# Kernel tuning notes

Hardware: AMD Instinct MI355X
Metric: run time of the kernel (lower is better)

Reference implementation:

```python
import jax, jax.numpy as jnp
import numpy as np
from jax.ops import segment_sum

N_NODES = 100000
N_EDGES = 3200000
N_GRAPHS = 64


def gcn_conv(x, src, dst, W, b, num_nodes):
    h = x @ W  # [N, H]
    loop = jnp.arange(num_nodes, dtype=src.dtype)
    s = jnp.concatenate([src, loop])
    d = jnp.concatenate([dst, loop])
    deg = segment_sum(jnp.ones_like(d, dtype=h.dtype), d, num_segments=num_nodes)
    dinv = jnp.where(deg > 0, jax.lax.rsqrt(deg), 0.0)
    norm = dinv[s] * dinv[d]  # [E+N]
    msgs = h[s] * norm[:, None]  # gather + scale
    out = segment_sum(msgs, d, num_segments=num_nodes)  # scatter-add to targets
    return out + b


def setup_inputs() -> dict:
    key = jax.random.key(0)
    ks = jax.random.split(key, 8)
    F_IN, H, C = 128, 256, 2
    x = jax.random.normal(ks[0], (N_NODES, F_IN), dtype=jnp.float32)
    edge_index = jax.random.randint(ks[1], (2, N_EDGES), 0, N_NODES, dtype=jnp.int64)
    batch = jnp.sort(jax.random.randint(ks[2], (N_NODES,), 0, N_GRAPHS, dtype=jnp.int64))
    W1 = jax.random.normal(ks[3], (F_IN, H), dtype=jnp.float32) / np.sqrt(F_IN)
    b1 = jnp.zeros((H,), dtype=jnp.float32)
    W2 = jax.random.normal(ks[4], (H, H), dtype=jnp.float32) / np.sqrt(H)
    b2 = jnp.zeros((H,), dtype=jnp.float32)
    fc_w = jax.random.normal(ks[5], (H, C), dtype=jnp.float32) / np.sqrt(H)
    fc_b = jnp.zeros((C,), dtype=jnp.float32)
    return {"x": x, "edge_index": edge_index, "batch": batch, "W1": W1, "b1": b1,
            "W2": W2, "b2": b2, "fc_w": fc_w, "fc_b": fc_b}


def reference(x, edge_index, batch, W1, b1, W2, b2, fc_w, fc_b):
    src, dst = edge_index[0], edge_index[1]
    n = x.shape[0]
    h = jax.nn.relu(gcn_conv(x, src, dst, W1, b1, n))
    h = jax.nn.relu(gcn_conv(h, src, dst, W2, b2, n))
    # global_mean_pool over graph ids
    sums = segment_sum(h, batch, num_segments=N_GRAPHS)  # [G, H]
    cnts = segment_sum(jnp.ones((n,), dtype=h.dtype), batch, num_segments=N_GRAPHS)
    pooled = sums / jnp.maximum(cnts, 1.0)[:, None]
    logits = pooled @ fc_w + fc_b
    return jax.nn.log_softmax(logits, axis=1)
```

## Files before the change

### kernel.cpp

```cpp
#include <hip/hip_runtime.h>
#include <cstdint>

#define N_NODES 100000
#define N_EDGES 3200000
#define N_GRAPHS 64
#define HDIM 256
#define F_IN 128

#define BUCKET_BITS 7
#define NPB 128
#define N_BUCKETS ((N_NODES + NPB - 1) / NPB)
#define CHUNK 8192
#define NCHUNK ((N_EDGES + CHUNK - 1) / CHUNK)

typedef __attribute__((ext_vector_type(8))) short bf16x8;
typedef __attribute__((ext_vector_type(4))) float f32x4;
typedef __attribute__((ext_vector_type(2))) float f32x2;

__device__ __forceinline__ unsigned short f2bf(float f) {
    unsigned int b = __float_as_uint(f);
    b = (b + 0x7FFFu + ((b >> 16) & 1u)) >> 16;
    return (unsigned short)b;
}

__device__ __forceinline__ unsigned int pack4_fp8(float a, float b, float c, float d) {
    int v = 0;
    v = __builtin_amdgcn_cvt_pk_fp8_f32(a, b, v, false);
    v = __builtin_amdgcn_cvt_pk_fp8_f32(c, d, v, true);
    return (unsigned int)v;
}
__device__ __forceinline__ unsigned char pack1_fp8(float a) {
    int v = __builtin_amdgcn_cvt_pk_fp8_f32(a, a, 0, false);
    return (unsigned char)(v & 0xFF);
}

__global__ void zero_f(float* p, int n) {
    int i = blockIdx.x * blockDim.x + threadIdx.x;
    if (i < n) p[i] = 0.0f;
}

__global__ __launch_bounds__(256) void block_count(const int* __restrict__ dst,
                                                   int* __restrict__ counts, int nE) {
    __shared__ int hist[N_BUCKETS];
    int blk = blockIdx.x, t = threadIdx.x;
    for (int i = t; i < N_BUCKETS; i += 256) hist[i] = 0;
    __syncthreads();
    int lo = blk * CHUNK;
    int hi = lo + CHUNK < nE ? lo + CHUNK : nE;
    for (int i = lo + t; i < hi; i += 256) atomicAdd(&hist[dst[i] >> BUCKET_BITS], 1);
    __syncthreads();
    for (int i = t; i < N_BUCKETS; i += 256) counts[blk * N_BUCKETS + i] = hist[i];
}

__global__ __launch_bounds__(256) void bucket_totals(const int* __restrict__ counts,
                                                     int* __restrict__ tot) {
    __shared__ int red[256];
    int b = blockIdx.x, t = threadIdx.x;
    int s = 0;
    for (int blk = t; blk < NCHUNK; blk += 256) s += counts[blk * N_BUCKETS + b];
    red[t] = s;
    __syncthreads();
    for (int o = 128; o > 0; o >>= 1) {
        if (t < o) red[t] += red[t + o];
        __syncthreads();
    }
    if (t == 0) tot[b] = red[0];
}

__global__ __launch_bounds__(1024) void scan_buckets(const int* __restrict__ tot,
                                                     int* __restrict__ base, int nb) {
    __shared__ int lds[1024];
    int t = threadIdx.x;
    int v = (t < nb) ? tot[t] : 0;
    lds[t] = v;
    __syncthreads();
    for (int off = 1; off < 1024; off <<= 1) {
        int a = (t >= off) ? lds[t - off] : 0;
        __syncthreads();
        lds[t] += a;
        __syncthreads();
    }
    int excl = lds[t] - v;
    if (t < nb) base[t] = excl;
    if (t == nb) base[t] = excl;
}

__global__ __launch_bounds__(512) void column_scan(const int* __restrict__ counts,
                                                   const int* __restrict__ base,
                                                   int* __restrict__ offs) {
    __shared__ int lds[512];
    int b = blockIdx.x, t = threadIdx.x;
    int v = (t < NCHUNK) ? counts[t * N_BUCKETS + b] : 0;
    lds[t] = v;
    __syncthreads();
    for (int off = 1; off < 512; off <<= 1) {
        int a = (t >= off) ? lds[t - off] : 0;
        __syncthreads();
        lds[t] += a;
        __syncthreads();
    }
    if (t < NCHUNK) offs[t * N_BUCKETS + b] = base[b] + lds[t] - v;
}

__global__ __launch_bounds__(256) void block_scatter(const int* __restrict__ src,
                                                     const int* __restrict__ dst,
                                                     const int* __restrict__ offs,
                                                     unsigned int* __restrict__ rec, int nE) {
    __shared__ int cur[N_BUCKETS];
    int blk = blockIdx.x, t = threadIdx.x;
    for (int i = t; i < N_BUCKETS; i += 256) cur[i] = offs[blk * N_BUCKETS + i];
    __syncthreads();
    int lo = blk * CHUNK;
    int hi = lo + CHUNK < nE ? lo + CHUNK : nE;
    for (int i = lo + t; i < hi; i += 256) {
        int d = dst[i];
        int b = d >> BUCKET_BITS;
        int pos = atomicAdd(&cur[b], 1);
        rec[pos] = (unsigned int)src[i] | ((unsigned int)(d & (NPB - 1)) << 17);
    }
}

__global__ __launch_bounds__(512) void bucket_csr(const unsigned int* __restrict__ rec,
                                                  const int* __restrict__ base,
                                                  int* __restrict__ ptr, float* __restrict__ dinv,
                                                  int* __restrict__ csr_src, int n) {
    __shared__ int hist[NPB];
    __shared__ int sc[NPB];
    __shared__ int cur[NPB];
    int b = blockIdx.x;
    int lo = base[b], hi = base[b + 1];
    int t = threadIdx.x;
    if (t < NPB) hist[t] = 0;
    __syncthreads();
    for (int i = lo + t; i < hi; i += 512) atomicAdd(&hist[rec[i] >> 17], 1);
    __syncthreads();
    if (t < NPB) sc[t] = hist[t];
    __syncthreads();
    for (int off = 1; off < NPB; off <<= 1) {
        int a = (t < NPB && t >= off) ? sc[t - off] : 0;
        __syncthreads();
        if (t < NPB) sc[t] += a;
        __syncthreads();
    }
    if (t < NPB) {
        int node = b * NPB + t;
        int incl = sc[t];
        int excl = incl - hist[t];
        if (node < n) {
            ptr[node] = lo + incl;
            dinv[node] = rsqrtf((float)hist[t] + 1.0f);
        }
        cur[t] = lo + excl;
    }
    __syncthreads();
    for (int i = lo + t; i < hi; i += 512) {
        unsigned int r = rec[i];
        int pos = atomicAdd(&cur[r >> 17], 1);
        csr_src[pos] = (int)(r & 0x1FFFFu);
    }
}

__global__ void convert_x_pre(const float* __restrict__ x, const float* __restrict__ dinv,
                              unsigned int* __restrict__ xp, int n) {
    int tid = blockIdx.x * blockDim.x + threadIdx.x;
    if (tid >= n * (F_IN / 4)) return;
    int node = tid / (F_IN / 4);
    float di = dinv[node];
    float4 v = ((const float4*)x)[tid];
    xp[tid] = pack4_fp8(v.x * di, v.y * di, v.z * di, v.w * di);
}

__global__ void pack_w(const float* __restrict__ W, unsigned short* __restrict__ hi,
                       unsigned short* __restrict__ lo, int K) {
    int idx = blockIdx.x * blockDim.x + threadIdx.x;
    if (idx >= K * HDIM) return;
    int k = idx >> 8, c = idx & 255;
    float w = W[idx];
    unsigned short h = f2bf(w);
    float hf = __uint_as_float((unsigned int)h << 16);
    unsigned short l = f2bf(w - hf);
    int pos = ((k >> 5) * 16 + (c >> 4)) * 512 + ((((k >> 3) & 3) * 16) + (c & 15)) * 8 + (k & 7);
    hi[pos] = h;
    lo[pos] = l;
}

__global__ void csr_agg128_fp8(const unsigned char* __restrict__ h, const int* __restrict__ ptr,
                               const int* __restrict__ csr, const float* __restrict__ dinv,
                               unsigned short* __restrict__ out, int n) {
    int wave = threadIdx.x >> 6, lane = threadIdx.x & 63;
    int node = blockIdx.x * 4 + wave;
    if (node >= n) return;
    int begin = node ? ptr[node - 1] : 0;
    int end = ptr[node];
    unsigned int u = *(const unsigned short*)(h + (size_t)node * 128 + lane * 2);
    f32x2 v = __builtin_amdgcn_cvt_pk_f32_fp8((int)u, false);
    float a0 = v.x, a1 = v.y;
    int i = begin;
    for (; i + 8 <= end; i += 8) {
        unsigned int uu[8];
#pragma unroll
        for (int j = 0; j < 8; j++) {
            int s = csr[i + j];
            uu[j] = *(const unsigned short*)(h + (size_t)s * 128 + lane * 2);
        }
#pragma unroll
        for (int j = 0; j < 8; j++) {
            f32x2 d = __builtin_amdgcn_cvt_pk_f32_fp8((int)uu[j], false);
            a0 += d.x; a1 += d.y;
        }
    }
    for (; i < end; i++) {
        int s = csr[i];
        unsigned int u0 = *(const unsigned short*)(h + (size_t)s * 128 + lane * 2);
        f32x2 d = __builtin_amdgcn_cvt_pk_f32_fp8((int)u0, false);
        a0 += d.x; a1 += d.y;
    }
    float dn = dinv[node];
    unsigned int o = (unsigned int)f2bf(a0 * dn) | ((unsigned int)f2bf(a1 * dn) << 16);
    *(unsigned int*)(out + (size_t)node * 128 + lane * 2) = o;
}

__global__ void csr_agg256_fp8(const unsigned char* __restrict__ h, const int* __restrict__ ptr,
                               const int* __restrict__ csr, const float* __restrict__ dinv,
                               unsigned short* __restrict__ out, int n) {
    int wave = threadIdx.x >> 6, lane = threadIdx.x & 63;
    int node = blockIdx.x * 4 + wave;
    if (node >= n) return;
    int begin = node ? ptr[node - 1] : 0;
    int end = ptr[node];
    unsigned int u = *(const unsigned int*)(h + (size_t)node * 256 + lane * 4);
    f32x2 vl = __builtin_amdgcn_cvt_pk_f32_fp8((int)u, false);
    f32x2 vh = __builtin_amdgcn_cvt_pk_f32_fp8((int)u, true);
    float a0 = vl.x, a1 = vl.y, a2 = vh.x, a3 = vh.y;
    int i = begin;
    for (; i + 8 <= end; i += 8) {
        unsigned int uu[8];
#pragma unroll
        for (int j = 0; j < 8; j++) {
            int s = csr[i + j];
            uu[j] = *(const unsigned int*)(h + (size_t)s * 256 + lane * 4);
        }
#pragma unroll
        for (int j = 0; j < 8; j++) {
            f32x2 dl = __builtin_amdgcn_cvt_pk_f32_fp8((int)uu[j], false);
            f32x2 dh = __builtin_amdgcn_cvt_pk_f32_fp8((int)uu[j], true);
            a0 += dl.x; a1 += dl.y; a2 += dh.x; a3 += dh.y;
        }
    }
    for (; i < end; i++) {
        int s = csr[i];
        unsigned int u0 = *(const unsigned int*)(h + (size_t)s * 256 + lane * 4);
        f32x2 dl = __builtin_amdgcn_cvt_pk_f32_fp8((int)u0, false);
        f32x2 dh = __builtin_amdgcn_cvt_pk_f32_fp8((int)u0, true);
        a0 += dl.x; a1 += dl.y; a2 += dh.x; a3 += dh.y;
    }
    float dn = dinv[node];
    uint2 o;
    o.x = (unsigned int)f2bf(a0 * dn) | ((unsigned int)f2bf(a1 * dn) << 16);
    o.y = (unsigned int)f2bf(a2 * dn) | ((unsigned int)f2bf(a3 * dn) << 16);
    *(uint2*)(out + (size_t)node * 256 + lane * 4) = o;
}

template <int K, bool PRESCALE>
__global__ __launch_bounds__(256, 3) void gemm_mfma(
    const unsigned short* __restrict__ A, const unsigned short* __restrict__ Whi,
    const unsigned short* __restrict__ Wlo, const float* __restrict__ bias,
    const float* __restrict__ dinv, void* __restrict__ outp, int n) {
    int wave = threadIdx.x >> 6, lane = threadIdx.x & 63;
    int quad = lane >> 4, l16 = lane & 15;
    int rowgrp = wave >> 1, colhalf = wave & 1;
    int rowbase = blockIdx.x * 64 + rowgrp * 32;

    f32x4 acc[2][8];
#pragma unroll
    for (int s = 0; s < 2; s++)
#pragma unroll
        for (int ct = 0; ct < 8; ct++) acc[s][ct] = (f32x4){0.f, 0.f, 0.f, 0.f};

    int r0 = rowbase + l16;
    int r1 = rowbase + 16 + l16;
    int rc0 = r0 < n ? r0 : n - 1;
    int rc1 = r1 < n ? r1 : n - 1;

    for (int kt = 0; kt < K / 32; kt++) {
        bf16x8 a0 = *(const bf16x8*)(A + (size_t)rc0 * K + kt * 32 + quad * 8);
        bf16x8 a1 = *(const bf16x8*)(A + (size_t)rc1 * K + kt * 32 + quad * 8);
        const unsigned short* wh = Whi + ((size_t)kt * 16 + colhalf * 8) * 512 + lane * 8;
        const unsigned short* wl = Wlo + ((size_t)kt * 16 + colhalf * 8) * 512 + lane * 8;
#pragma unroll
        for (int ct = 0; ct < 8; ct++) {
            bf16x8 bh = *(const bf16x8*)(wh + ct * 512);
            bf16x8 bl = *(const bf16x8*)(wl + ct * 512);
            acc[0][ct] = __builtin_amdgcn_mfma_f32_16x16x32_bf16(a0, bh, acc[0][ct], 0, 0, 0);
            acc[0][ct] = __builtin_amdgcn_mfma_f32_16x16x32_bf16(a0, bl, acc[0][ct], 0, 0, 0);
            acc[1][ct] = __builtin_amdgcn_mfma_f32_16x16x32_bf16(a1, bh, acc[1][ct], 0, 0, 0);
            acc[1][ct] = __builtin_amdgcn_mfma_f32_16x16x32_bf16(a1, bl, acc[1][ct], 0, 0, 0);
        }
    }

#pragma unroll
    for (int s = 0; s < 2; s++) {
#pragma unroll
        for (int ct = 0; ct < 8; ct++) {
            int col = colhalf * 128 + ct * 16 + l16;
            float b = bias[col];
#pragma unroll
            for (int r = 0; r < 4; r++) {
                int row = rowbase + s * 16 + quad * 4 + r;
                if (row < n) {
                    float v = acc[s][ct][r] + b;
                    v = v > 0.0f ? v : 0.0f;
                    if (PRESCALE) {
                        ((unsigned char*)outp)[(size_t)row * HDIM + col] = pack1_fp8(v * dinv[row]);
                    } else {
                        ((float*)outp)[(size_t)row * HDIM + col] = v;
                    }
                }
            }
        }
    }
}

__global__ void pool_sum_runs(const float* __restrict__ h, const int* __restrict__ batch,
                              float* __restrict__ pool, float* __restrict__ cnt, int n) {
    constexpr int ROWS = 128;
    int f = threadIdx.x;
    int r0 = blockIdx.x * ROWS;
    int rend = r0 + ROWS;
    if (rend > n) rend = n;
    float acc = 0.0f;
    int cur = batch[r0];
    int runlen = 0;
    for (int r = r0; r < rend; r++) {
        int g = batch[r];
        if (g != cur) {
            atomicAdd(&pool[cur * HDIM + f], acc);
            if (f == 0) atomicAdd(&cnt[cur], (float)runlen);
            acc = 0.0f; runlen = 0; cur = g;
        }
        acc += h[(size_t)r * HDIM + f];
        runlen++;
    }
    atomicAdd(&pool[cur * HDIM + f], acc);
    if (f == 0) atomicAdd(&cnt[cur], (float)runlen);
}

__global__ void final_head(const float* __restrict__ pool, const float* __restrict__ cnt,
                           const float* __restrict__ fcw, const float* __restrict__ fcb,
                           float* __restrict__ out) {
    int g = threadIdx.x;
    if (g < N_GRAPHS) {
        float c = cnt[g];
        c = c > 1.0f ? c : 1.0f;
        float inv = 1.0f / c;
        float l0 = fcb[0], l1 = fcb[1];
        for (int f = 0; f < HDIM; f++) {
            float p = pool[g * HDIM + f] * inv;
            l0 += p * fcw[f * 2 + 0];
            l1 += p * fcw[f * 2 + 1];
        }
        float m = fmaxf(l0, l1);
        float lse = m + logf(expf(l0 - m) + expf(l1 - m));
        out[g * 2 + 0] = l0 - lse;
        out[g * 2 + 1] = l1 - lse;
    }
}

extern "C" void kernel_launch(void* const* d_in, const int* in_sizes, int n_in,
                              void* d_out, int out_size, void* d_ws, size_t ws_size,
                              hipStream_t stream) {
    const float* x = (const float*)d_in[0];
    const int* ei = (const int*)d_in[1];
    const int* batch = (const int*)d_in[2];
    const float* W1 = (const float*)d_in[3];
    const float* b1 = (const float*)d_in[4];
    const float* W2 = (const float*)d_in[5];
    const float* b2 = (const float*)d_in[6];
    const float* fcw = (const float*)d_in[7];
    const float* fcb = (const float*)d_in[8];
    float* out = (float*)d_out;

    const int* src = ei;
    const int* dst = ei + N_EDGES;

    char* ws = (char*)d_ws;
    float* dinv = (float*)ws;            ws += 4 * ((N_NODES + 255) & ~255);
    int* ptr = (int*)ws;                 ws += 4 * ((N_NODES + 255) & ~255);
    int* csr_src = (int*)ws;             ws += 4 * (size_t)N_EDGES;
    int* counts = (int*)ws;              ws += 4 * (size_t)NCHUNK * N_BUCKETS;
    int* offs = (int*)ws;                ws += 4 * (size_t)NCHUNK * N_BUCKETS;
    int* tot = (int*)ws;                 ws += 4 * 1024;
    int* bbase = (int*)ws;               ws += 4 * 1024;
    unsigned short* W1hi = (unsigned short*)ws; ws += 2 * F_IN * HDIM;
    unsigned short* W1lo = (unsigned short*)ws; ws += 2 * F_IN * HDIM;
    unsigned short* W2hi = (unsigned short*)ws; ws += 2 * HDIM * HDIM;
    unsigned short* W2lo = (unsigned short*)ws; ws += 2 * HDIM * HDIM;
    float* pool = (float*)ws;            ws += 4 * N_GRAPHS * HDIM;
    float* cnt = (float*)ws;             ws += 4 * ((N_GRAPHS + 63) & ~63);
    char* R0 = ws;                       ws += 4 * (size_t)N_NODES * HDIM;
    unsigned char* x_pre = (unsigned char*)R0;
    unsigned short* A1 = (unsigned short*)(R0 + (size_t)N_NODES * F_IN);
    unsigned char* h1_pre = (unsigned char*)(R0 + 3 * (size_t)N_NODES * F_IN);
    float* h2 = (float*)R0;
    unsigned short* A2 = (unsigned short*)ws;
    unsigned int* records = (unsigned int*)A2;

    block_count<<<NCHUNK, 256, 0, stream>>>(dst, counts, N_EDGES);
    bucket_totals<<<N_BUCKETS, 256, 0, stream>>>(counts, tot);
    scan_buckets<<<1, 1024, 0, stream>>>(tot, bbase, N_BUCKETS);
    column_scan<<<N_BUCKETS, 512, 0, stream>>>(counts, bbase, offs);
    block_scatter<<<NCHUNK, 256, 0, stream>>>(src, dst, offs, records, N_EDGES);
    bucket_csr<<<N_BUCKETS, 512, 0, stream>>>(records, bbase, ptr, dinv, csr_src, N_NODES);

    convert_x_pre<<<(N_NODES * (F_IN / 4) + 255) / 256, 256, 0, stream>>>(
        x, dinv, (unsigned int*)x_pre, N_NODES);
    pack_w<<<(F_IN * HDIM + 255) / 256, 256, 0, stream>>>(W1, W1hi, W1lo, F_IN);
    pack_w<<<(HDIM * HDIM + 255) / 256, 256, 0, stream>>>(W2, W2hi, W2lo, HDIM);

    csr_agg128_fp8<<<(N_NODES + 3) / 4, 256, 0, stream>>>(x_pre, ptr, csr_src, dinv, A1, N_NODES);
    gemm_mfma<F_IN, true><<<(N_NODES + 63) / 64, 256, 0, stream>>>(A1, W1hi, W1lo, b1, dinv,
                                                                   h1_pre, N_NODES);
    csr_agg256_fp8<<<(N_NODES + 3) / 4, 256, 0, stream>>>(h1_pre, ptr, csr_src, dinv, A2, N_NODES);
    gemm_mfma<HDIM, false><<<(N_NODES + 63) / 64, 256, 0, stream>>>(A2, W2hi, W2lo, b2, dinv,
                                                                    h2, N_NODES);

    zero_f<<<(N_GRAPHS * HDIM + N_GRAPHS + 255) / 256, 256, 0, stream>>>(
        pool, N_GRAPHS * HDIM + N_GRAPHS);
    pool_sum_runs<<<(N_NODES + 127) / 128, 256, 0, stream>>>(h2, batch, pool, cnt, N_NODES);
    final_head<<<1, 64, 0, stream>>>(pool, cnt, fcw, fcb, out);
}
```

Before: 661.8 us.

## Fuse mean-pool into layer-2 GEMM epilogue and deepen gather unroll in aggregation

The layer-2 GEMM no longer writes the full fp32 hidden matrix to global memory. Its epilogue now accumulates ReLU outputs into per-graph sums, using shared-memory slots with spill to global atomics, so the separate pooling kernel and the h2 round trip through memory go away. Graph node counts are now found by binary search over the sorted batch vector inside the head kernel. The CSR aggregation loops now issue 16 gathers per batch, with a 4-wide remainder loop and packed float2 accumulation, to keep more loads in flight. The fused epilogue adds many shared and global atomics and relies on the batch vector being sorted.

```diff
diff --git a/kernel.cpp b/kernel.cpp
--- a/kernel.cpp
+++ b/kernel.cpp
@@ -193,30 +193,37 @@
     int begin = node ? ptr[node - 1] : 0;
     int end = ptr[node];
     unsigned int u = *(const unsigned short*)(h + (size_t)node * 128 + lane * 2);
-    f32x2 v = __builtin_amdgcn_cvt_pk_f32_fp8((int)u, false);
-    float a0 = v.x, a1 = v.y;
+    f32x2 a01 = __builtin_amdgcn_cvt_pk_f32_fp8((int)u, false);
     int i = begin;
-    for (; i + 8 <= end; i += 8) {
-        unsigned int uu[8];
-#pragma unroll
-        for (int j = 0; j < 8; j++) {
+    for (; i + 16 <= end; i += 16) {
+        unsigned int uu[16];
+#pragma unroll
+        for (int j = 0; j < 16; j++) {
             int s = csr[i + j];
             uu[j] = *(const unsigned short*)(h + (size_t)s * 128 + lane * 2);
         }
 #pragma unroll
-        for (int j = 0; j < 8; j++) {
-            f32x2 d = __builtin_amdgcn_cvt_pk_f32_fp8((int)uu[j], false);
-            a0 += d.x; a1 += d.y;
-        }
+        for (int j = 0; j < 16; j++)
+            a01 += __builtin_amdgcn_cvt_pk_f32_fp8((int)uu[j], false);
+    }
+    for (; i + 4 <= end; i += 4) {
+        unsigned int uu[4];
+#pragma unroll
+        for (int j = 0; j < 4; j++) {
+            int s = csr[i + j];
+            uu[j] = *(const unsigned short*)(h + (size_t)s * 128 + lane * 2);
+        }
+#pragma unroll
+        for (int j = 0; j < 4; j++)
+            a01 += __builtin_amdgcn_cvt_pk_f32_fp8((int)uu[j], false);
     }
     for (; i < end; i++) {
         int s = csr[i];
         unsigned int u0 = *(const unsigned short*)(h + (size_t)s * 128 + lane * 2);
-        f32x2 d = __builtin_amdgcn_cvt_pk_f32_fp8((int)u0, false);
-        a0 += d.x; a1 += d.y;
+        a01 += __builtin_amdgcn_cvt_pk_f32_fp8((int)u0, false);
     }
     float dn = dinv[node];
-    unsigned int o = (unsigned int)f2bf(a0 * dn) | ((unsigned int)f2bf(a1 * dn) << 16);
+    unsigned int o = (unsigned int)f2bf(a01.x * dn) | ((unsigned int)f2bf(a01.y * dn) << 16);
     *(unsigned int*)(out + (size_t)node * 128 + lane * 2) = o;
 }
 
@@ -229,47 +236,65 @@
     int begin = node ? ptr[node - 1] : 0;
     int end = ptr[node];
     unsigned int u = *(const unsigned int*)(h + (size_t)node * 256 + lane * 4);
-    f32x2 vl = __builtin_amdgcn_cvt_pk_f32_fp8((int)u, false);
-    f32x2 vh = __builtin_amdgcn_cvt_pk_f32_fp8((int)u, true);
-    float a0 = vl.x, a1 = vl.y, a2 = vh.x, a3 = vh.y;
+    f32x2 a01 = __builtin_amdgcn_cvt_pk_f32_fp8((int)u, false);
+    f32x2 a23 = __builtin_amdgcn_cvt_pk_f32_fp8((int)u, true);
     int i = begin;
-    for (; i + 8 <= end; i += 8) {
-        unsigned int uu[8];
-#pragma unroll
-        for (int j = 0; j < 8; j++) {
+    for (; i + 16 <= end; i += 16) {
+        unsigned int uu[16];
+#pragma unroll
+        for (int j = 0; j < 16; j++) {
             int s = csr[i + j];
             uu[j] = *(const unsigned int*)(h + (size_t)s * 256 + lane * 4);
         }
 #pragma unroll
-        for (int j = 0; j < 8; j++) {
-            f32x2 dl = __builtin_amdgcn_cvt_pk_f32_fp8((int)uu[j], false);
-            f32x2 dh = __builtin_amdgcn_cvt_pk_f32_fp8((int)uu[j], true);
-            a0 += dl.x; a1 += dl.y; a2 += dh.x; a3 += dh.y;
+        for (int j = 0; j < 16; j++) {
+            a01 += __builtin_amdgcn_cvt_pk_f32_fp8((int)uu[j], false);
+            a23 += __builtin_amdgcn_cvt_pk_f32_fp8((int)uu[j], true);
+        }
+    }
+    for (; i + 4 <= end; i += 4) {
+        unsigned int uu[4];
+#pragma unroll
+        for (int j = 0; j < 4; j++) {
+            int s = csr[i + j];
+            uu[j] = *(const unsigned int*)(h + (size_t)s * 256 + lane * 4);
+        }
+#pragma unroll
+        for (int j = 0; j < 4; j++) {
+            a01 += __builtin_amdgcn_cvt_pk_f32_fp8((int)uu[j], false);
+            a23 += __builtin_amdgcn_cvt_pk_f32_fp8((int)uu[j], true);
         }
     }
     for (; i < end; i++) {
         int s = csr[i];
         unsigned int u0 = *(const unsigned int*)(h + (size_t)s * 256 + lane * 4);
-        f32x2 dl = __builtin_amdgcn_cvt_pk_f32_fp8((int)u0, false);
-        f32x2 dh = __builtin_amdgcn_cvt_pk_f32_fp8((int)u0, true);
-        a0 += dl.x; a1 += dl.y; a2 += dh.x; a3 += dh.y;
+        a01 += __builtin_amdgcn_cvt_pk_f32_fp8((int)u0, false);
+        a23 += __builtin_amdgcn_cvt_pk_f32_fp8((int)u0, true);
     }
     float dn = dinv[node];
     uint2 o;
-    o.x = (unsigned int)f2bf(a0 * dn) | ((unsigned int)f2bf(a1 * dn) << 16);
-    o.y = (unsigned int)f2bf(a2 * dn) | ((unsigned int)f2bf(a3 * dn) << 16);
+    o.x = (unsigned int)f2bf(a01.x * dn) | ((unsigned int)f2bf(a01.y * dn) << 16);
+    o.y = (unsigned int)f2bf(a23.x * dn) | ((unsigned int)f2bf(a23.y * dn) << 16);
     *(uint2*)(out + (size_t)node * 256 + lane * 4) = o;
 }
 
-template <int K, bool PRESCALE>
+template <int K, int MODE>
 __global__ __launch_bounds__(256, 3) void gemm_mfma(
     const unsigned short* __restrict__ A, const unsigned short* __restrict__ Whi,
     const unsigned short* __restrict__ Wlo, const float* __restrict__ bias,
-    const float* __restrict__ dinv, void* __restrict__ outp, int n) {
+    const float* __restrict__ dinv, const int* __restrict__ batch,
+    float* __restrict__ pool, void* __restrict__ outp, int n) {
+    __shared__ float lpool[4 * 256];
     int wave = threadIdx.x >> 6, lane = threadIdx.x & 63;
     int quad = lane >> 4, l16 = lane & 15;
     int rowgrp = wave >> 1, colhalf = wave & 1;
-    int rowbase = blockIdx.x * 64 + rowgrp * 32;
+    int blockrow = blockIdx.x * 64;
+    int rowbase = blockrow + rowgrp * 32;
+
+    if (MODE == 1) {
+        for (int i = threadIdx.x; i < 4 * 256; i += 256) lpool[i] = 0.0f;
+        __syncthreads();
+    }
 
     f32x4 acc[2][8];
 #pragma unroll
@@ -298,61 +323,80 @@
         }
     }
 
-#pragma unroll
-    for (int s = 0; s < 2; s++) {
-#pragma unroll
-        for (int ct = 0; ct < 8; ct++) {
-            int col = colhalf * 128 + ct * 16 + l16;
-            float b = bias[col];
-#pragma unroll
-            for (int r = 0; r < 4; r++) {
-                int row = rowbase + s * 16 + quad * 4 + r;
-                if (row < n) {
-                    float v = acc[s][ct][r] + b;
-                    v = v > 0.0f ? v : 0.0f;
-                    if (PRESCALE) {
+    if (MODE == 0) {
+#pragma unroll
+        for (int s = 0; s < 2; s++) {
+#pragma unroll
+            for (int ct = 0; ct < 8; ct++) {
+                int col = colhalf * 128 + ct * 16 + l16;
+                float b = bias[col];
+#pragma unroll
+                for (int r = 0; r < 4; r++) {
+                    int row = rowbase + s * 16 + quad * 4 + r;
+                    if (row < n) {
+                        float v = acc[s][ct][r] + b;
+                        v = v > 0.0f ? v : 0.0f;
                         ((unsigned char*)outp)[(size_t)row * HDIM + col] = pack1_fp8(v * dinv[row]);
-                    } else {
-                        ((float*)outp)[(size_t)row * HDIM + col] = v;
                     }
                 }
             }
         }
-    }
-}
-
-__global__ void pool_sum_runs(const float* __restrict__ h, const int* __restrict__ batch,
-                              float* __restrict__ pool, float* __restrict__ cnt, int n) {
-    constexpr int ROWS = 128;
-    int f = threadIdx.x;
-    int r0 = blockIdx.x * ROWS;
-    int rend = r0 + ROWS;
-    if (rend > n) rend = n;
-    float acc = 0.0f;
-    int cur = batch[r0];
-    int runlen = 0;
-    for (int r = r0; r < rend; r++) {
-        int g = batch[r];
-        if (g != cur) {
-            atomicAdd(&pool[cur * HDIM + f], acc);
-            if (f == 0) atomicAdd(&cnt[cur], (float)runlen);
-            acc = 0.0f; runlen = 0; cur = g;
-        }
-        acc += h[(size_t)r * HDIM + f];
-        runlen++;
-    }
-    atomicAdd(&pool[cur * HDIM + f], acc);
-    if (f == 0) atomicAdd(&cnt[cur], (float)runlen);
-}
-
-__global__ void final_head(const float* __restrict__ pool, const float* __restrict__ cnt,
+    } else {
+        int g0 = batch[blockrow < n ? blockrow : n - 1];
+        int gr[2][4];
+#pragma unroll
+        for (int s = 0; s < 2; s++)
+#pragma unroll
+            for (int r = 0; r < 4; r++) {
+                int row = rowbase + s * 16 + quad * 4 + r;
+                gr[s][r] = (row < n) ? batch[row] : -1;
+            }
+#pragma unroll
+        for (int s = 0; s < 2; s++) {
+#pragma unroll
+            for (int ct = 0; ct < 8; ct++) {
+                int col = colhalf * 128 + ct * 16 + l16;
+                float b = bias[col];
+#pragma unroll
+                for (int r = 0; r < 4; r++) {
+                    int g = gr[s][r];
+                    if (g >= 0) {
+                        float v = acc[s][ct][r] + b;
+                        v = v > 0.0f ? v : 0.0f;
+                        int slot = g - g0;
+                        if (slot < 4) {
+                            atomicAdd(&lpool[slot * 256 + col], v);
+                        } else {
+                            atomicAdd(&pool[g * HDIM + col], v);
+                        }
+                    }
+                }
+            }
+        }
+        __syncthreads();
+        for (int i = threadIdx.x; i < 4 * 256; i += 256) {
+            float val = lpool[i];
+            if (val != 0.0f) {
+                int slot = i >> 8, col = i & 255;
+                atomicAdd(&pool[(g0 + slot) * HDIM + col], val);
+            }
+        }
+    }
+}
+
+__global__ void final_head(const float* __restrict__ pool, const int* __restrict__ batch,
                            const float* __restrict__ fcw, const float* __restrict__ fcb,
-                           float* __restrict__ out) {
+                           float* __restrict__ out, int n) {
     int g = threadIdx.x;
     if (g < N_GRAPHS) {
-        float c = cnt[g];
-        c = c > 1.0f ? c : 1.0f;
-        float inv = 1.0f / c;
+        int lo = 0, hi = n;
+        while (lo < hi) { int m = (lo + hi) >> 1; if (batch[m] < g) lo = m + 1; else hi = m; }
+        int b0 = lo;
+        lo = 0; hi = n;
+        while (lo < hi) { int m = (lo + hi) >> 1; if (batch[m] < g + 1) lo = m + 1; else hi = m; }
+        int c = lo - b0;
+        float cf = c > 1 ? (float)c : 1.0f;
+        float inv = 1.0f / cf;
         float l0 = fcb[0], l1 = fcb[1];
         for (int f = 0; f < HDIM; f++) {
             float p = pool[g * HDIM + f] * inv;
@@ -396,12 +440,10 @@
     unsigned short* W2hi = (unsigned short*)ws; ws += 2 * HDIM * HDIM;
     unsigned short* W2lo = (unsigned short*)ws; ws += 2 * HDIM * HDIM;
     float* pool = (float*)ws;            ws += 4 * N_GRAPHS * HDIM;
-    float* cnt = (float*)ws;             ws += 4 * ((N_GRAPHS + 63) & ~63);
     char* R0 = ws;                       ws += 4 * (size_t)N_NODES * HDIM;
     unsigned char* x_pre = (unsigned char*)R0;
     unsigned short* A1 = (unsigned short*)(R0 + (size_t)N_NODES * F_IN);
     unsigned char* h1_pre = (unsigned char*)(R0 + 3 * (size_t)N_NODES * F_IN);
-    float* h2 = (float*)R0;
     unsigned short* A2 = (unsigned short*)ws;
     unsigned int* records = (unsigned int*)A2;
 
@@ -416,16 +458,14 @@
         x, dinv, (unsigned int*)x_pre, N_NODES);
     pack_w<<<(F_IN * HDIM + 255) / 256, 256, 0, stream>>>(W1, W1hi, W1lo, F_IN);
     pack_w<<<(HDIM * HDIM + 255) / 256, 256, 0, stream>>>(W2, W2hi, W2lo, HDIM);
+    zero_f<<<(N_GRAPHS * HDIM + 255) / 256, 256, 0, stream>>>(pool, N_GRAPHS * HDIM);
 
     csr_agg128_fp8<<<(N_NODES + 3) / 4, 256, 0, stream>>>(x_pre, ptr, csr_src, dinv, A1, N_NODES);
-    gemm_mfma<F_IN, true><<<(N_NODES + 63) / 64, 256, 0, stream>>>(A1, W1hi, W1lo, b1, dinv,
-                                                                   h1_pre, N_NODES);
+    gemm_mfma<F_IN, 0><<<(N_NODES + 63) / 64, 256, 0, stream>>>(A1, W1hi, W1lo, b1, dinv,
+                                                                nullptr, nullptr, h1_pre, N_NODES);
     csr_agg256_fp8<<<(N_NODES + 3) / 4, 256, 0, stream>>>(h1_pre, ptr, csr_src, dinv, A2, N_NODES);
-    gemm_mfma<HDIM, false><<<(N_NODES + 63) / 64, 256, 0, stream>>>(A2, W2hi, W2lo, b2, dinv,
-                                                                    h2, N_NODES);
-
-    zero_f<<<(N_GRAPHS * HDIM + N_GRAPHS + 255) / 256, 256, 0, stream>>>(
-        pool, N_GRAPHS * HDIM + N_GRAPHS);
-    pool_sum_runs<<<(N_NODES + 127) / 128, 256, 0, stream>>>(h2, batch, pool, cnt, N_NODES);
-    final_head<<<1, 64, 0, stream>>>(pool, cnt, fcw, fcb, out);
-}
+    gemm_mfma<HDIM, 1><<<(N_NODES + 63) / 64, 256, 0, stream>>>(A2, W2hi, W2lo, b2, dinv,
+                                                                batch, pool, nullptr, N_NODES);
+
+    final_head<<<1, 64, 0, stream>>>(pool, batch, fcw, fcb, out, N_NODES);
+}
```

Measured after the change: 733.3 us. 10.8% more time.
